# Kernel tuning notes

Hardware: AMD Instinct MI355X
Metric: run time of the kernel (lower is better)

The kernel has to match this reference:

```python
import jax, jax.numpy as jnp
import numpy as np

B, S, D = 4, 4096, 256
UNITS = 256
NRF = 256  # n_random_features (must equal units for the score matmul)


def setup_inputs() -> dict:
    key = jax.random.key(0)
    ks = jax.random.split(key, 10)
    s = 1.0 / np.sqrt(D)
    return {
        "query": jax.random.normal(ks[0], (B, S, D), jnp.float32),
        "value": jax.random.normal(ks[1], (B, S, D), jnp.float32),
        "Wq": jax.random.normal(ks[2], (D, UNITS), jnp.float32) * s,
        "bq": jnp.zeros((UNITS,), jnp.float32),
        "Wk": jax.random.normal(ks[3], (D, UNITS), jnp.float32) * s,
        "bk": jnp.zeros((UNITS,), jnp.float32),
        "Wv": jax.random.normal(ks[4], (D, UNITS), jnp.float32) * s,
        "bv": jnp.zeros((UNITS,), jnp.float32),
        # random-feature map params (non-trainable in original, init 'random_normal' ~ stddev 0.05)
        "Wr": jax.random.normal(ks[5], (UNITS, NRF), jnp.float32) * 0.05,
        "br": jax.random.normal(ks[6], (NRF,), jnp.float32) * 0.05,
    }


def reference(query, value, Wq, bq, Wk, bk, Wv, bv, Wr, br):
    # Dense projections
    Q = jnp.einsum("bsd,du->bsu", query, Wq) + bq   # [B,S,U]
    K = jnp.einsum("bsd,du->bsu", value, Wk) + bk   # [B,S,U]
    V = jnp.einsum("bsd,du->bsu", value, Wv) + bv   # [B,S,U]
    # random-feature kernel map on K
    K_hat = jnp.cos(jnp.einsum("bsu,ur->bsr", K, Wr) + br)  # [B,S,R]
    # attention: Q @ K_hat^T -> softmax -> @ V
    scores = jnp.einsum("bqr,bkr->bqk", Q, K_hat)    # [B,S,S]
    probs = jax.nn.softmax(scores, axis=-1)
    return jnp.einsum("bqk,bku->bqu", probs, V)      # [B,S,U]
```

## Files before the change

kernel.cpp:

```cpp
#include <hip/hip_runtime.h>
#include <hip/hip_bf16.h>

typedef _Float16 f16;
typedef _Float16 f16x8 __attribute__((ext_vector_type(8)));
typedef _Float16 f16x4 __attribute__((ext_vector_type(4)));
typedef float f32x4 __attribute__((ext_vector_type(4)));
typedef float f32x16 __attribute__((ext_vector_type(16)));

#define MFMA1632(a, b, c) __builtin_amdgcn_mfma_f32_16x16x32_f16(a, b, c, 0, 0, 0)
#define MFMA3216(a, b, c) __builtin_amdgcn_mfma_f32_32x32x16_f16(a, b, c, 0, 0, 0)

#define GLL16(g, l)                                                        \
    __builtin_amdgcn_global_load_lds(                                      \
        (const __attribute__((address_space(1))) void*)(g),                \
        (__attribute__((address_space(3))) void*)(l), 16, 0, 0)

static constexpr int S  = 4096;
static constexpr int NB = 4;

__global__ void wconv4_kernel(const float* __restrict__ W0, const float* __restrict__ W1,
                              const float* __restrict__ W2, const float* __restrict__ W3,
                              f16* __restrict__ T0, f16* __restrict__ T1,
                              f16* __restrict__ T2, f16* __restrict__ T3) {
    int j = blockIdx.x >> 8;
    int k = blockIdx.x & 255;
    int n = threadIdx.x;
    const float* W = (j == 0) ? W0 : (j == 1) ? W1 : (j == 2) ? W2 : W3;
    f16*         T = (j == 0) ? T0 : (j == 1) ? T1 : (j == 2) ? T2 : T3;
    T[n * 256 + k] = (f16)W[k * 256 + n];
}

__global__ __launch_bounds__(512) void kvhproj_kernel(
    const float* __restrict__ Af,
    const f16* __restrict__ WkT, const f16* __restrict__ WvT,
    const f16* __restrict__ WrT,
    const float* __restrict__ bk, const float* __restrict__ bv,
    const float* __restrict__ br,
    f16* __restrict__ Hf, f16* __restrict__ VtF)
{
    __shared__ f16 KS[32][264];

    int mbase = blockIdx.x * 32;
    int tid = threadIdx.x;
    int w = tid >> 6, l = tid & 63;
    int lr = l & 15, lg = l >> 4;
    int path = w >> 2;
    int nbase = (w & 3) * 64;
    const f16* Wt = path ? WvT : WkT;
    const float* bias = path ? bv : bk;

    f32x4 acc[2][4];
#pragma unroll
    for (int mf = 0; mf < 2; ++mf)
#pragma unroll
        for (int nf = 0; nf < 4; ++nf) acc[mf][nf] = f32x4{0.f, 0.f, 0.f, 0.f};

#pragma unroll
    for (int ks = 0; ks < 8; ++ks) {
        int kof = ks * 32 + lg * 8;
        f16x8 a[2], b[4];
#pragma unroll
        for (int mf = 0; mf < 2; ++mf) {
            int row = mbase + mf * 16 + lr;
            const float4* p = (const float4*)(Af + row * 256 + kof);
            float4 x0 = p[0], x1 = p[1];
            f16x8 t;
            t[0] = (f16)x0.x; t[1] = (f16)x0.y; t[2] = (f16)x0.z; t[3] = (f16)x0.w;
            t[4] = (f16)x1.x; t[5] = (f16)x1.y; t[6] = (f16)x1.z; t[7] = (f16)x1.w;
            a[mf] = t;
        }
#pragma unroll
        for (int nf = 0; nf < 4; ++nf) {
            int col = nbase + nf * 16 + lr;
            b[nf] = *(const f16x8*)(Wt + col * 256 + kof);
        }
#pragma unroll
        for (int mf = 0; mf < 2; ++mf)
#pragma unroll
            for (int nf = 0; nf < 4; ++nf)
                acc[mf][nf] = MFMA1632(a[mf], b[nf], acc[mf][nf]);
    }

#pragma unroll
    for (int mf = 0; mf < 2; ++mf) {
#pragma unroll
        for (int nf = 0; nf < 4; ++nf) {
            int col = nbase + nf * 16 + lr;
            float bv2 = bias[col];
            if (path == 0) {
#pragma unroll
                for (int r = 0; r < 4; ++r)
                    KS[mf * 16 + lg * 4 + r][col] = (f16)(acc[mf][nf][r] + bv2);
            } else {
                int bi = mbase >> 12;
                int s  = (mbase & (S - 1)) + mf * 16 + lg * 4;
                f16x4 v;
#pragma unroll
                for (int r = 0; r < 4; ++r) v[r] = (f16)(acc[mf][nf][r] + bv2);
                *(f16x4*)(VtF + ((bi * 256 + col) * S + s)) = v;
            }
        }
    }
    __syncthreads();

    f32x4 acc2[2][2];
#pragma unroll
    for (int mf = 0; mf < 2; ++mf)
#pragma unroll
        for (int nf = 0; nf < 2; ++nf) acc2[mf][nf] = f32x4{0.f, 0.f, 0.f, 0.f};

#pragma unroll
    for (int ks = 0; ks < 8; ++ks) {
        int kof = ks * 32 + lg * 8;
        f16x8 a[2], b[2];
#pragma unroll
        for (int mf = 0; mf < 2; ++mf)
            a[mf] = *(const f16x8*)&KS[mf * 16 + lr][kof];
#pragma unroll
        for (int nf = 0; nf < 2; ++nf) {
            int col = w * 32 + nf * 16 + lr;
            b[nf] = *(const f16x8*)(WrT + col * 256 + kof);
        }
#pragma unroll
        for (int mf = 0; mf < 2; ++mf)
#pragma unroll
            for (int nf = 0; nf < 2; ++nf)
                acc2[mf][nf] = MFMA1632(a[mf], b[nf], acc2[mf][nf]);
    }

#pragma unroll
    for (int mf = 0; mf < 2; ++mf) {
#pragma unroll
        for (int nf = 0; nf < 2; ++nf) {
            int col = w * 32 + nf * 16 + lr;
            float bv2 = br[col];
#pragma unroll
            for (int r = 0; r < 4; ++r) {
                int row = mbase + mf * 16 + lg * 4 + r;
                Hf[row * 256 + col] = (f16)cosf(acc2[mf][nf][r] + bv2);
            }
        }
    }
}

__global__ __launch_bounds__(512, 2) void attn_kernel(
    const float* __restrict__ query, const f16* __restrict__ WqT,
    const float* __restrict__ bq,
    const f16* __restrict__ Hf, const f16* __restrict__ Vt,
    float* __restrict__ Out)
{
    __shared__ f16 KhS[128 * 256];
    __shared__ f16 VtS[256 * 128];
    __shared__ f16 PSh[64 * 128];
    __shared__ float auxF[2][4][32];
    __shared__ float auxT[2][32];
    __shared__ float auxC[2][32];
    __shared__ int flagLds;

    int bid = blockIdx.x;
    int b   = (bid >> 1) & 3;
    int qi  = ((bid >> 3) << 1) | (bid & 1);
    int qbase = qi * 64;

    int tid = threadIdx.x;
    int w  = tid >> 6, l = tid & 63;
    int qh = w >> 2;
    int kg = w & 3;
    int lm = l & 31;
    int h  = l >> 5;

    const f16* Hbase = Hf + (size_t)b * S * 256;
    const f16* Vbase = Vt + (size_t)b * 256 * S;

    if (tid == 0) flagLds = 0;

    f16 (*QS)[264] = (f16(*)[264])VtS;
    {
        int lr = l & 15, lg = l >> 4;
        int mh = w >> 2;
        int nc = (w & 3) * 64;
        const float* Abase = query + (size_t)(b * S + qbase + mh * 32) * 256;

        f32x4 acc[2][4];
#pragma unroll
        for (int mf = 0; mf < 2; ++mf)
#pragma unroll
            for (int nf = 0; nf < 4; ++nf) acc[mf][nf] = f32x4{0.f, 0.f, 0.f, 0.f};

#pragma unroll
        for (int ks = 0; ks < 8; ++ks) {
            int kof = ks * 32 + lg * 8;
            f16x8 a[2], bb[4];
#pragma unroll
            for (int mf = 0; mf < 2; ++mf) {
                const float4* p = (const float4*)(Abase + (size_t)(mf * 16 + lr) * 256 + kof);
                float4 x0 = p[0], x1 = p[1];
                f16x8 t;
                t[0] = (f16)x0.x; t[1] = (f16)x0.y; t[2] = (f16)x0.z; t[3] = (f16)x0.w;
                t[4] = (f16)x1.x; t[5] = (f16)x1.y; t[6] = (f16)x1.z; t[7] = (f16)x1.w;
                a[mf] = t;
            }
#pragma unroll
            for (int nf = 0; nf < 4; ++nf) {
                int col = nc + nf * 16 + lr;
                bb[nf] = *(const f16x8*)(WqT + col * 256 + kof);
            }
#pragma unroll
            for (int mf = 0; mf < 2; ++mf)
#pragma unroll
                for (int nf = 0; nf < 4; ++nf)
                    acc[mf][nf] = MFMA1632(a[mf], bb[nf], acc[mf][nf]);
        }
#pragma unroll
        for (int mf = 0; mf < 2; ++mf) {
#pragma unroll
            for (int nf = 0; nf < 4; ++nf) {
                int col = nc + nf * 16 + lr;
                float bv = bq[col];
#pragma unroll
                for (int r = 0; r < 4; ++r)
                    QS[mh * 32 + mf * 16 + lg * 4 + r][col] = (f16)(acc[mf][nf][r] + bv);
            }
        }
    }
    __syncthreads();

    f16x8 qf[16];
    {
        const f16* qp = &QS[qh * 32 + lm][h * 8];
#pragma unroll
        for (int s = 0; s < 16; ++s) qf[s] = *(const f16x8*)(qp + s * 16);
    }
    __syncthreads();

    f32x16 oac0, oac1;
#pragma unroll
    for (int i = 0; i < 16; ++i) { oac0[i] = 0.f; oac1[i] = 0.f; }
    float mrun = -1e30f, lsum = 0.f;

#pragma unroll
    for (int i = 0; i < 8; ++i) {
        int c = i * 512 + tid;
        int row = c >> 5, ch = c & 31;
        GLL16(Hbase + (size_t)row * 256 + ((ch ^ (row & 31)) * 8),
              KhS + (size_t)(i * 4096 + w * 512));
    }
#pragma unroll
    for (int i = 0; i < 8; ++i) {
        int d  = w * 32 + i * 4 + (l >> 4);
        int cp = l & 15;
        GLL16(Vbase + (size_t)d * S + ((cp ^ (d & 15)) * 8),
              VtS + (size_t)(w * 4096 + i * 512));
    }
    __syncthreads();

    const int NT = S / 128;
    for (int t = 0; t < NT; ++t) {
        int kt = t * 128;

        f32x16 s0, s1;
#pragma unroll
        for (int i = 0; i < 16; ++i) { s0[i] = 0.f; s1[i] = 0.f; }
        {
            const f16* kb = KhS + (size_t)(kg * 32 + lm) * 256;
            __builtin_amdgcn_s_setprio(1);
#pragma unroll
            for (int s = 0; s < 16; s += 2) {
                f16x8 ka0 = *(const f16x8*)(kb + ((2 * s + h) ^ lm) * 8);
                f16x8 ka1 = *(const f16x8*)(kb + ((2 * s + 2 + h) ^ lm) * 8);
                s0 = MFMA3216(ka0, qf[s], s0);
                s1 = MFMA3216(ka1, qf[s + 1], s1);
            }
            __builtin_amdgcn_s_setprio(0);
        }
        f32x16 sc;
#pragma unroll
        for (int i = 0; i < 16; ++i) sc[i] = s0[i] + s1[i];

        int need = 0;
#pragma unroll
        for (int i = 0; i < 16; ++i) need |= (sc[i] > mrun + 8.f) ? 1 : 0;
        if (__any(need)) { if (l == 0) flagLds = 1; }
        __syncthreads();

        if (t + 1 < NT) {
#pragma unroll
            for (int i = 0; i < 8; ++i) {
                int c = i * 512 + tid;
                int row = c >> 5, ch = c & 31;
                GLL16(Hbase + (size_t)(kt + 128 + row) * 256 + ((ch ^ (row & 31)) * 8),
                      KhS + (size_t)(i * 4096 + w * 512));
            }
        }

        if (flagLds) {
            float mx = sc[0];
#pragma unroll
            for (int i = 1; i < 16; ++i) mx = fmaxf(mx, sc[i]);
            mx = fmaxf(mx, __shfl_xor(mx, 32));
            if (l < 32) auxF[qh][kg][lm] = mx;
            __syncthreads();
            float mnew = fmaxf(fmaxf(auxF[qh][0][lm], auxF[qh][1][lm]),
                               fmaxf(auxF[qh][2][lm], auxF[qh][3][lm]));
            mnew = fmaxf(mrun, mnew);
            float corr = __expf(mrun - mnew);
            lsum *= corr;
            if (kg == 0 && l < 32) auxT[qh][lm] = corr;
            mrun = mnew;
            if (tid == 0) flagLds = 0;
            __syncthreads();
#pragma unroll
            for (int i = 0; i < 16; ++i) {
                int cr = (i & 3) + 8 * (i >> 2) + 4 * h;
                oac0[i] *= auxT[0][cr];
                oac1[i] *= auxT[1][cr];
            }
        }

        {
            f16* pw = PSh + (size_t)(qh * 32 + lm) * 128;
            int key = lm & 15;
#pragma unroll
            for (int b4 = 0; b4 < 4; ++b4) {
                float p0 = __expf(sc[b4 * 4 + 0] - mrun);
                float p1 = __expf(sc[b4 * 4 + 1] - mrun);
                float p2 = __expf(sc[b4 * 4 + 2] - mrun);
                float p3 = __expf(sc[b4 * 4 + 3] - mrun);
                lsum += (p0 + p1) + (p2 + p3);
                f16x4 pv;
                pv[0] = (f16)p0; pv[1] = (f16)p1; pv[2] = (f16)p2; pv[3] = (f16)p3;
                *(f16x4*)(pw + ((4 * kg + b4) ^ key) * 8 + 4 * h) = pv;
            }
        }

        asm volatile("s_waitcnt lgkmcnt(0)" ::: "memory");
        __builtin_amdgcn_s_barrier();

        {
            const f16* pb0 = PSh + (size_t)lm * 128;
            const f16* pb1 = PSh + (size_t)(32 + lm) * 128;
            const f16* vb  = VtS + (size_t)(w * 32 + lm) * 128;
            int kp = lm & 15;
            __builtin_amdgcn_s_setprio(1);
#pragma unroll
            for (int s = 0; s < 8; ++s) {
                int lc = 2 * s + h;
                f16x8 pa0 = *(const f16x8*)(pb0 + (lc ^ kp) * 8);
                f16x8 pa1 = *(const f16x8*)(pb1 + (lc ^ kp) * 8);
                f16x8 vv  = *(const f16x8*)(vb  + (lc ^ kp) * 8);
                oac0 = MFMA3216(pa0, vv, oac0);
                oac1 = MFMA3216(pa1, vv, oac1);
            }
            __builtin_amdgcn_s_setprio(0);
        }

        if (t + 1 < NT) {
#pragma unroll
            for (int i = 0; i < 8; ++i) {
                int d  = w * 32 + i * 4 + (l >> 4);
                int cp = l & 15;
                GLL16(Vbase + (size_t)d * S + (kt + 128) + ((cp ^ (d & 15)) * 8),
                      VtS + (size_t)(w * 4096 + i * 512));
            }
        }

        asm volatile("s_waitcnt vmcnt(8)" ::: "memory");
        __builtin_amdgcn_s_barrier();
    }

    lsum += __shfl_xor(lsum, 32);
    if (l < 32) auxF[qh][kg][lm] = lsum;
    __syncthreads();
    if (kg == 0 && l < 32) {
        float dsum = auxF[qh][0][lm] + auxF[qh][1][lm] +
                     auxF[qh][2][lm] + auxF[qh][3][lm];
        auxC[qh][lm] = 1.0f / dsum;
    }
    __syncthreads();

    float* Ob = Out + (size_t)(b * S + qbase) * 256 + w * 32 + lm;
#pragma unroll
    for (int i = 0; i < 16; ++i) {
        int cr = (i & 3) + 8 * (i >> 2) + 4 * h;
        Ob[(size_t)cr * 256]        = oac0[i] * auxC[0][cr];
        Ob[(size_t)(32 + cr) * 256] = oac1[i] * auxC[1][cr];
    }
}

extern "C" void kernel_launch(void* const* d_in, const int* in_sizes, int n_in,
                              void* d_out, int out_size, void* d_ws, size_t ws_size,
                              hipStream_t stream)
{
    const float* query = (const float*)d_in[0];
    const float* value = (const float*)d_in[1];
    const float* Wq    = (const float*)d_in[2];
    const float* bq    = (const float*)d_in[3];
    const float* Wk    = (const float*)d_in[4];
    const float* bk    = (const float*)d_in[5];
    const float* Wv    = (const float*)d_in[6];
    const float* bv    = (const float*)d_in[7];
    const float* Wr    = (const float*)d_in[8];
    const float* br    = (const float*)d_in[9];
    float* out = (float*)d_out;

    char* ws = (char*)d_ws;
    size_t off = 0;
    auto alloc = [&](size_t bytes) -> char* {
        char* p = ws + off;
        off += (bytes + 255) & ~(size_t)255;
        return p;
    };
    f16* WqT = (f16*)alloc((size_t)65536 * 2);
    f16* WkT = (f16*)alloc((size_t)65536 * 2);
    f16* WvT = (f16*)alloc((size_t)65536 * 2);
    f16* WrT = (f16*)alloc((size_t)65536 * 2);
    f16* Hf  = (f16*)alloc((size_t)NB * S * 256 * 2);
    f16* VtF = (f16*)alloc((size_t)NB * S * 256 * 2);
    (void)ws_size; (void)in_sizes; (void)n_in; (void)out_size;

    wconv4_kernel<<<1024, 256, 0, stream>>>(Wq, Wk, Wv, Wr, WqT, WkT, WvT, WrT);

    kvhproj_kernel<<<512, 512, 0, stream>>>(value, WkT, WvT, WrT, bk, bv, br, Hf, VtF);

    attn_kernel<<<256, 512, 0, stream>>>(query, WqT, bq, Hf, VtF, out);
}
```

Measured before the change: 160.0 us.

## Double-buffer K-hat tiles in LDS and read V directly from global

Replaces the single K-hat and V LDS buffers with a double-buffered K-hat tile. The next tile's prefetch is issued at the top of each iteration, which removes one full barrier before the prefetch. V fragments for the PV MFMA are now loaded straight from global memory per wave rather than staged through LDS. The Q staging area moves into the second K buffer, and the first K tile load is issued before the Q projection so the two overlap. The risk is that uncoalesced global V loads sit on the MFMA critical path, and the vmcnt(0) wait drains all outstanding loads every iteration.

```diff
diff --git a/kernel.cpp b/kernel.cpp
--- a/kernel.cpp
+++ b/kernel.cpp
@@ -149,8 +149,7 @@
     const f16* __restrict__ Hf, const f16* __restrict__ Vt,
     float* __restrict__ Out)
 {
-    __shared__ f16 KhS[128 * 256];
-    __shared__ f16 VtS[256 * 128];
+    __shared__ f16 KhS[2][128 * 256];
     __shared__ f16 PSh[64 * 128];
     __shared__ float auxF[2][4][32];
     __shared__ float auxT[2][32];
@@ -174,7 +173,15 @@
 
     if (tid == 0) flagLds = 0;
 
-    f16 (*QS)[264] = (f16(*)[264])VtS;
+#pragma unroll
+    for (int i = 0; i < 8; ++i) {
+        int c = i * 512 + tid;
+        int row = c >> 5, ch = c & 31;
+        GLL16(Hbase + (size_t)row * 256 + ((ch ^ (row & 31)) * 8),
+              &KhS[0][(size_t)(i * 4096 + w * 512)]);
+    }
+
+    f16 (*QS)[264] = (f16(*)[264])&KhS[1][0];
     {
         int lr = l & 15, lg = l >> 4;
         int mh = w >> 2;
@@ -238,31 +245,26 @@
     for (int i = 0; i < 16; ++i) { oac0[i] = 0.f; oac1[i] = 0.f; }
     float mrun = -1e30f, lsum = 0.f;
 
-#pragma unroll
-    for (int i = 0; i < 8; ++i) {
-        int c = i * 512 + tid;
-        int row = c >> 5, ch = c & 31;
-        GLL16(Hbase + (size_t)row * 256 + ((ch ^ (row & 31)) * 8),
-              KhS + (size_t)(i * 4096 + w * 512));
-    }
-#pragma unroll
-    for (int i = 0; i < 8; ++i) {
-        int d  = w * 32 + i * 4 + (l >> 4);
-        int cp = l & 15;
-        GLL16(Vbase + (size_t)d * S + ((cp ^ (d & 15)) * 8),
-              VtS + (size_t)(w * 4096 + i * 512));
-    }
-    __syncthreads();
-
     const int NT = S / 128;
     for (int t = 0; t < NT; ++t) {
+        int cur = t & 1;
         int kt = t * 128;
+
+        if (t + 1 < NT) {
+#pragma unroll
+            for (int i = 0; i < 8; ++i) {
+                int c = i * 512 + tid;
+                int row = c >> 5, ch = c & 31;
+                GLL16(Hbase + (size_t)(kt + 128 + row) * 256 + ((ch ^ (row & 31)) * 8),
+                      &KhS[cur ^ 1][(size_t)(i * 4096 + w * 512)]);
+            }
+        }
 
         f32x16 s0, s1;
 #pragma unroll
         for (int i = 0; i < 16; ++i) { s0[i] = 0.f; s1[i] = 0.f; }
         {
-            const f16* kb = KhS + (size_t)(kg * 32 + lm) * 256;
+            const f16* kb = &KhS[cur][(size_t)(kg * 32 + lm) * 256];
             __builtin_amdgcn_s_setprio(1);
 #pragma unroll
             for (int s = 0; s < 16; s += 2) {
@@ -281,17 +283,8 @@
 #pragma unroll
         for (int i = 0; i < 16; ++i) need |= (sc[i] > mrun + 8.f) ? 1 : 0;
         if (__any(need)) { if (l == 0) flagLds = 1; }
-        __syncthreads();
-
-        if (t + 1 < NT) {
-#pragma unroll
-            for (int i = 0; i < 8; ++i) {
-                int c = i * 512 + tid;
-                int row = c >> 5, ch = c & 31;
-                GLL16(Hbase + (size_t)(kt + 128 + row) * 256 + ((ch ^ (row & 31)) * 8),
-                      KhS + (size_t)(i * 4096 + w * 512));
-            }
-        }
+        asm volatile("s_waitcnt lgkmcnt(0)" ::: "memory");
+        __builtin_amdgcn_s_barrier();
 
         if (flagLds) {
             float mx = sc[0];
@@ -339,7 +332,7 @@
         {
             const f16* pb0 = PSh + (size_t)lm * 128;
             const f16* pb1 = PSh + (size_t)(32 + lm) * 128;
-            const f16* vb  = VtS + (size_t)(w * 32 + lm) * 128;
+            const f16* vb  = Vbase + (size_t)(w * 32 + lm) * S + kt;
             int kp = lm & 15;
             __builtin_amdgcn_s_setprio(1);
 #pragma unroll
@@ -347,24 +340,14 @@
                 int lc = 2 * s + h;
                 f16x8 pa0 = *(const f16x8*)(pb0 + (lc ^ kp) * 8);
                 f16x8 pa1 = *(const f16x8*)(pb1 + (lc ^ kp) * 8);
-                f16x8 vv  = *(const f16x8*)(vb  + (lc ^ kp) * 8);
+                f16x8 vv  = *(const f16x8*)(vb + lc * 8);
                 oac0 = MFMA3216(pa0, vv, oac0);
                 oac1 = MFMA3216(pa1, vv, oac1);
             }
             __builtin_amdgcn_s_setprio(0);
         }
 
-        if (t + 1 < NT) {
-#pragma unroll
-            for (int i = 0; i < 8; ++i) {
-                int d  = w * 32 + i * 4 + (l >> 4);
-                int cp = l & 15;
-                GLL16(Vbase + (size_t)d * S + (kt + 128) + ((cp ^ (d & 15)) * 8),
-                      VtS + (size_t)(w * 4096 + i * 512));
-            }
-        }
-
-        asm volatile("s_waitcnt vmcnt(8)" ::: "memory");
+        asm volatile("s_waitcnt vmcnt(0)" ::: "memory");
         __builtin_amdgcn_s_barrier();
     }
 
```

Result: slower. 199.4 us (+24.6%).
